# Kernel tuning notes

Measured on AMD Instinct MI355X. Metric: run time of the kernel, lower is better.

Reference implementation:

```python
import jax, jax.numpy as jnp
import numpy as np

HEAD_DIM = 64  # scale = head_dim ** -0.5


def setup_inputs() -> dict:
    key = jax.random.key(0)
    ks = jax.random.split(key, 5)
    B, S, E = 8, 8192, 1024
    L, D = 64, 256          # n_latent_vec, latent_dim
    H = HEAD_DIM
    return {
        "input_tensor": jax.random.normal(ks[0], (B, S, E), dtype=jnp.float32),
        "latents": jax.random.normal(ks[1], (L, D), dtype=jnp.float32),
        "Wq": jax.random.normal(ks[2], (H, D), dtype=jnp.float32) * (1.0 / np.sqrt(D)),
        "Wk": jax.random.normal(ks[3], (H, E), dtype=jnp.float32) * (1.0 / np.sqrt(E)),
        "Wv": jax.random.normal(ks[4], (H, E), dtype=jnp.float32) * (1.0 / np.sqrt(E)),
    }


def reference(input_tensor, latents, Wq, Wk, Wv):
    # non-cached path, seq_len == max_seq_len so no truncation
    # queries: broadcast shared latents over batch -> [B, L, H]
    q = jnp.einsum('ld,hd->lh', latents, Wq)                 # [L, H]
    k = jnp.einsum('bse,he->bsh', input_tensor, Wk)           # [B, S, H]
    v = jnp.einsum('bse,he->bsh', input_tensor, Wv)           # [B, S, H]
    scale = HEAD_DIM ** -0.5
    scores = jnp.einsum('lh,bsh->bls', q, k) * scale          # [B, L, S]
    weights = jax.nn.softmax(scores, axis=-1)                 # dropout is identity (p=0 / eval)
    out = jnp.einsum('bls,bsh->blh', weights, v)              # [B, L, H]
    return out
```

## Files before the change

kernel.cpp:

```cpp
#include <hip/hip_runtime.h>
#include <stdint.h>


typedef __attribute__((__ext_vector_type__(4))) float f32x4;
typedef __attribute__((__ext_vector_type__(8))) short bf16x8;

__device__ __forceinline__ unsigned short f2bf(float f) {
    union { float f; uint32_t u; } v; v.f = f;
    uint32_t u = v.u;
    return (unsigned short)((u + 0x7fffu + ((u >> 16) & 1u)) >> 16);
}

__device__ __forceinline__ unsigned long long pack4(f32x4 v) {
    return (unsigned long long)f2bf(v[0])        |
           ((unsigned long long)f2bf(v[1]) << 16) |
           ((unsigned long long)f2bf(v[2]) << 32) |
           ((unsigned long long)f2bf(v[3]) << 48);
}

__global__ __launch_bounds__(256) void prep_kernel(
    const float* __restrict__ latents, const float* __restrict__ Wq,
    const float* __restrict__ Wk, const float* __restrict__ Wv,
    unsigned short* __restrict__ wkv, unsigned short* __restrict__ qbf)
{
    const int blk = blockIdx.x, tid = threadIdx.x;
    if (blk < 128) {
        const float* src = (blk < 64) ? (Wk + (size_t)blk * 1024)
                                      : (Wv + (size_t)(blk - 64) * 1024);
        for (int i = tid; i < 1024; i += 256)
            wkv[(size_t)blk * 1024 + i] = f2bf(src[i]);
    } else {
        const int l = (blk - 128) * 4 + (tid >> 6);
        const int h = tid & 63;
        float a = 0.f;
        #pragma unroll 8
        for (int d = 0; d < 256; ++d)
            a += latents[l * 256 + d] * Wq[h * 256 + d];
        qbf[l * 64 + h] = f2bf(a * 0.125f);
    }
}

__global__ __launch_bounds__(512, 4) void fused_kernel(
    const float* __restrict__ x, const unsigned short* __restrict__ wkv,
    const unsigned short* __restrict__ qbf,
    float* __restrict__ Opart, float* __restrict__ mpart, float* __restrict__ spart)
{
    __shared__ unsigned short smem[33792];
    unsigned short* Ab = smem;
    unsigned short* Bb = smem + 10240;
    unsigned short* Cs = smem;
    unsigned short* qs = smem + 20480;
    unsigned short* Ps = smem + 25088;
    __shared__ float red[4][64];
    __shared__ float Mrow[64];

    const int tid = threadIdx.x;
    const int wave = tid >> 6, lane = tid & 63;
    const int g = lane >> 4, c = lane & 15;
    const int wr = wave >> 2, wc = wave & 3;
    const size_t r0 = (size_t)blockIdx.x * 128;

    {
        const int rowQ = tid >> 3, colQ = (tid & 7) * 8;
        *(uint4*)&qs[rowQ * 72 + colQ] = *(const uint4*)(qbf + rowQ * 64 + colQ);
    }

    const int rowA = tid >> 3, colA = (tid & 7) * 4;
    const int rowB = tid >> 2, colB = (tid & 3) * 8;

    f32x4 acc[4][2];
    #pragma unroll
    for (int i = 0; i < 4; ++i)
        #pragma unroll
        for (int j = 0; j < 2; ++j)
            acc[i][j] = f32x4{0.f, 0.f, 0.f, 0.f};

    f32x4 areg[2];
    uint4  breg;

    #pragma unroll
    for (int i = 0; i < 2; ++i)
        areg[i] = *(const f32x4*)(x + (r0 + rowA + 64 * i) * 1024 + colA);
    breg = *(const uint4*)(wkv + (size_t)rowB * 1024 + colB);
    #pragma unroll
    for (int i = 0; i < 2; ++i)
        *(unsigned long long*)&Ab[(rowA + 64 * i) * 40 + colA] = pack4(areg[i]);
    *(uint4*)&Bb[rowB * 40 + colB] = breg;
    __syncthreads();

    for (int t = 0; t < 32; ++t) {
        const int buf = t & 1;
        if (t < 31) {
            const int e0 = (t + 1) * 32;
            #pragma unroll
            for (int i = 0; i < 2; ++i)
                areg[i] = *(const f32x4*)(x + (r0 + rowA + 64 * i) * 1024 + e0 + colA);
            breg = *(const uint4*)(wkv + (size_t)rowB * 1024 + e0 + colB);
        }
        bf16x8 af[4], bfr[2];
        #pragma unroll
        for (int ml = 0; ml < 4; ++ml)
            af[ml] = *(const bf16x8*)&Ab[(buf * 128 + 64 * wr + 16 * ml + c) * 40 + 8 * g];
        #pragma unroll
        for (int nc = 0; nc < 2; ++nc)
            bfr[nc] = *(const bf16x8*)&Bb[(buf * 128 + 32 * wc + 16 * nc + c) * 40 + 8 * g];
        #pragma unroll
        for (int ml = 0; ml < 4; ++ml)
            #pragma unroll
            for (int nc = 0; nc < 2; ++nc)
                acc[ml][nc] = __builtin_amdgcn_mfma_f32_16x16x32_bf16(
                    af[ml], bfr[nc], acc[ml][nc], 0, 0, 0);
        if (t < 31) {
            const int nb = buf ^ 1;
            #pragma unroll
            for (int i = 0; i < 2; ++i)
                *(unsigned long long*)&Ab[(nb * 128 + rowA + 64 * i) * 40 + colA] =
                    pack4(areg[i]);
            *(uint4*)&Bb[(nb * 128 + rowB) * 40 + colB] = breg;
        }
        __syncthreads();
    }

    #pragma unroll
    for (int ml = 0; ml < 4; ++ml)
        #pragma unroll
        for (int nc = 0; nc < 2; ++nc)
            #pragma unroll
            for (int r = 0; r < 4; ++r)
                Cs[(64 * wr + 16 * ml + 4 * g + r) * 136 + 32 * wc + 16 * nc + c] =
                    f2bf(acc[ml][nc][r]);
    __syncthreads();

    f32x4 sc[4][2];
    if (wave < 4) {
        #pragma unroll
        for (int ml = 0; ml < 4; ++ml)
            #pragma unroll
            for (int ns = 0; ns < 2; ++ns)
                sc[ml][ns] = f32x4{0.f, 0.f, 0.f, 0.f};
        #pragma unroll
        for (int k0 = 0; k0 < 2; ++k0) {
            bf16x8 aq[4];
            #pragma unroll
            for (int ml = 0; ml < 4; ++ml)
                aq[ml] = *(const bf16x8*)&qs[(16 * ml + c) * 72 + 32 * k0 + 8 * g];
            #pragma unroll
            for (int ns = 0; ns < 2; ++ns) {
                bf16x8 bk = *(const bf16x8*)&Cs[(32 * wave + 16 * ns + c) * 136 + 32 * k0 + 8 * g];
                #pragma unroll
                for (int ml = 0; ml < 4; ++ml)
                    sc[ml][ns] = __builtin_amdgcn_mfma_f32_16x16x32_bf16(
                        aq[ml], bk, sc[ml][ns], 0, 0, 0);
            }
        }
        float mloc[4][4];
        #pragma unroll
        for (int ml = 0; ml < 4; ++ml)
            #pragma unroll
            for (int r = 0; r < 4; ++r)
                mloc[ml][r] = fmaxf(sc[ml][0][r], sc[ml][1][r]);
        #pragma unroll
        for (int off = 1; off <= 8; off <<= 1)
            #pragma unroll
            for (int ml = 0; ml < 4; ++ml)
                #pragma unroll
                for (int r = 0; r < 4; ++r)
                    mloc[ml][r] = fmaxf(mloc[ml][r], __shfl_xor(mloc[ml][r], off));
        if (c == 0)
            #pragma unroll
            for (int ml = 0; ml < 4; ++ml)
                #pragma unroll
                for (int r = 0; r < 4; ++r)
                    red[wave][16 * ml + 4 * g + r] = mloc[ml][r];
    }
    __syncthreads();
    if (tid < 64) {
        float m = red[0][tid];
        m = fmaxf(m, red[1][tid]); m = fmaxf(m, red[2][tid]); m = fmaxf(m, red[3][tid]);
        Mrow[tid] = m;
    }
    __syncthreads();

    if (wave < 4) {
        float ssum[4][4];
        #pragma unroll
        for (int ml = 0; ml < 4; ++ml)
            #pragma unroll
            for (int r = 0; r < 4; ++r)
                ssum[ml][r] = 0.f;
        #pragma unroll
        for (int ml = 0; ml < 4; ++ml)
            #pragma unroll
            for (int r = 0; r < 4; ++r) {
                const int l = 16 * ml + 4 * g + r;
                const float mr = Mrow[l];
                #pragma unroll
                for (int ns = 0; ns < 2; ++ns) {
                    float p = __expf(sc[ml][ns][r] - mr);
                    unsigned short pb = f2bf(p);
                    Ps[l * 136 + 32 * wave + 16 * ns + c] = pb;
                    union { uint32_t u; float f; } pv; pv.u = (uint32_t)pb << 16;
                    ssum[ml][r] += pv.f;
                }
            }
        #pragma unroll
        for (int off = 1; off <= 8; off <<= 1)
            #pragma unroll
            for (int ml = 0; ml < 4; ++ml)
                #pragma unroll
                for (int r = 0; r < 4; ++r)
                    ssum[ml][r] += __shfl_xor(ssum[ml][r], off);
        if (c == 0)
            #pragma unroll
            for (int ml = 0; ml < 4; ++ml)
                #pragma unroll
                for (int r = 0; r < 4; ++r)
                    red[wave][16 * ml + 4 * g + r] = ssum[ml][r];
    }
    __syncthreads();
    if (tid < 64) {
        const float s = red[0][tid] + red[1][tid] + red[2][tid] + red[3][tid];
        mpart[(size_t)blockIdx.x * 64 + tid] = Mrow[tid];
        spart[(size_t)blockIdx.x * 64 + tid] = s;
    }

    if (wave < 4) {
        f32x4 o[4];
        #pragma unroll
        for (int nh = 0; nh < 4; ++nh) o[nh] = f32x4{0.f, 0.f, 0.f, 0.f};
        #pragma unroll
        for (int ks = 0; ks < 4; ++ks) {
            bf16x8 ap = *(const bf16x8*)&Ps[(16 * wave + c) * 136 + 32 * ks + 8 * g];
            #pragma unroll
            for (int nh = 0; nh < 4; ++nh) {
                bf16x8 bv;
                #pragma unroll
                for (int j = 0; j < 8; ++j)
                    bv[j] = (short)Cs[(32 * ks + 8 * g + j) * 136 + 64 + 16 * nh + c];
                o[nh] = __builtin_amdgcn_mfma_f32_16x16x32_bf16(ap, bv, o[nh], 0, 0, 0);
            }
        }
        const size_t pb = (size_t)blockIdx.x * 64;
        #pragma unroll
        for (int nh = 0; nh < 4; ++nh)
            #pragma unroll
            for (int r = 0; r < 4; ++r) {
                const int l = 16 * wave + 4 * g + r;
                const int h = 16 * nh + c;
                Opart[(pb + l) * 64 + h] = o[nh][r];
            }
    }
}

__global__ __launch_bounds__(64) void combine_kernel(
    const float* __restrict__ Opart, const float* __restrict__ mpart,
    const float* __restrict__ spart, float* __restrict__ out)
{
    const int b = blockIdx.x >> 6, l = blockIdx.x & 63, h = threadIdx.x;
    float M = -3.0e38f;
    #pragma unroll 8
    for (int ch = 0; ch < 64; ++ch)
        M = fmaxf(M, mpart[((size_t)(b * 64 + ch)) * 64 + l]);
    float den = 0.f, acc = 0.f;
    #pragma unroll 8
    for (int ch = 0; ch < 64; ++ch) {
        const size_t idx = ((size_t)(b * 64 + ch)) * 64 + l;
        const float w = __expf(mpart[idx] - M);
        den += w * spart[idx];
        acc += w * Opart[idx * 64 + h];
    }
    out[((size_t)blockIdx.x) * 64 + h] = acc / den;
}

extern "C" void kernel_launch(void* const* d_in, const int* in_sizes, int n_in,
                              void* d_out, int out_size, void* d_ws, size_t ws_size,
                              hipStream_t stream)
{
    const float* x       = (const float*)d_in[0];
    const float* latents = (const float*)d_in[1];
    const float* Wq      = (const float*)d_in[2];
    const float* Wk      = (const float*)d_in[3];
    const float* Wv      = (const float*)d_in[4];
    float* out = (float*)d_out;
    char* ws = (char*)d_ws;

    unsigned short* wkv = (unsigned short*)(ws);
    unsigned short* qbf = (unsigned short*)(ws + 262144);
    float* Opart = (float*)(ws + 270336);
    float* mpart = (float*)(ws + 270336 + 8388608);
    float* spart = (float*)(ws + 270336 + 8388608 + 131072);

    hipLaunchKernelGGL(prep_kernel, dim3(144), dim3(256), 0, stream,
                       latents, Wq, Wk, Wv, wkv, qbf);
    hipLaunchKernelGGL(fused_kernel, dim3(512), dim3(512), 0, stream,
                       x, wkv, qbf, Opart, mpart, spart);
    hipLaunchKernelGGL(combine_kernel, dim3(512), dim3(64), 0, stream,
                       Opart, mpart, spart, out);
}
```

Measured before the change: 81.85 us.

## Halve fused block tile to 64 rows, read K/V weights directly from global

Each fused block now handles 64 sequence rows with 256 threads instead of 128 rows with 512 threads, which doubles the grid to 1024 blocks and the number of partial results the combine kernel merges. The bf16 Wk/Wv fragments are loaded straight from global memory (expected to hit cache) rather than staged through shared memory, and the K and V tiles are written into a shared buffer in two phases so shared memory shrinks sharply. The aim is higher occupancy and a better fill of the CUs, and all four waves now do useful work in the attention phase. In exchange, each block rereads the full weight matrix from cache, and the partial-result traffic and combine work double.

```diff
diff --git a/kernel.cpp b/kernel.cpp
--- a/kernel.cpp
+++ b/kernel.cpp
@@ -40,139 +40,121 @@
     }
 }
 
-__global__ __launch_bounds__(512, 4) void fused_kernel(
+__global__ __launch_bounds__(256, 4) void fused_kernel(
     const float* __restrict__ x, const unsigned short* __restrict__ wkv,
     const unsigned short* __restrict__ qbf,
     float* __restrict__ Opart, float* __restrict__ mpart, float* __restrict__ spart)
 {
-    __shared__ unsigned short smem[33792];
-    unsigned short* Ab = smem;
-    unsigned short* Bb = smem + 10240;
-    unsigned short* Cs = smem;
-    unsigned short* qs = smem + 20480;
-    unsigned short* Ps = smem + 25088;
+    __shared__ unsigned short smem[9856];
+    unsigned short* KV  = smem;
+    unsigned short* PsQ = smem + 4608;
+    unsigned short* Ab  = smem;
     __shared__ float red[4][64];
     __shared__ float Mrow[64];
 
     const int tid = threadIdx.x;
     const int wave = tid >> 6, lane = tid & 63;
     const int g = lane >> 4, c = lane & 15;
-    const int wr = wave >> 2, wc = wave & 3;
-    const size_t r0 = (size_t)blockIdx.x * 128;
-
-    {
-        const int rowQ = tid >> 3, colQ = (tid & 7) * 8;
-        *(uint4*)&qs[rowQ * 72 + colQ] = *(const uint4*)(qbf + rowQ * 64 + colQ);
-    }
-
-    const int rowA = tid >> 3, colA = (tid & 7) * 4;
-    const int rowB = tid >> 2, colB = (tid & 3) * 8;
-
-    f32x4 acc[4][2];
-    #pragma unroll
-    for (int i = 0; i < 4; ++i)
-        #pragma unroll
-        for (int j = 0; j < 2; ++j)
+    const int wr = wave >> 1, wc = wave & 1;
+    const size_t r0 = (size_t)blockIdx.x * 64;
+
+    const int rowS = tid >> 2, c4 = (tid & 3) * 4;
+
+    f32x4 acc[2][4];
+    #pragma unroll
+    for (int i = 0; i < 2; ++i)
+        #pragma unroll
+        for (int j = 0; j < 4; ++j)
             acc[i][j] = f32x4{0.f, 0.f, 0.f, 0.f};
 
-    f32x4 areg[2];
-    uint4  breg;
-
-    #pragma unroll
-    for (int i = 0; i < 2; ++i)
-        areg[i] = *(const f32x4*)(x + (r0 + rowA + 64 * i) * 1024 + colA);
-    breg = *(const uint4*)(wkv + (size_t)rowB * 1024 + colB);
-    #pragma unroll
-    for (int i = 0; i < 2; ++i)
-        *(unsigned long long*)&Ab[(rowA + 64 * i) * 40 + colA] = pack4(areg[i]);
-    *(uint4*)&Bb[rowB * 40 + colB] = breg;
+    f32x4 a0, a1;
+
+    a0 = *(const f32x4*)(x + (r0 + rowS) * 1024 + c4);
+    a1 = *(const f32x4*)(x + (r0 + rowS) * 1024 + c4 + 16);
+    *(unsigned long long*)&Ab[rowS * 40 + c4]      = pack4(a0);
+    *(unsigned long long*)&Ab[rowS * 40 + c4 + 16] = pack4(a1);
     __syncthreads();
 
     for (int t = 0; t < 32; ++t) {
         const int buf = t & 1;
         if (t < 31) {
             const int e0 = (t + 1) * 32;
-            #pragma unroll
-            for (int i = 0; i < 2; ++i)
-                areg[i] = *(const f32x4*)(x + (r0 + rowA + 64 * i) * 1024 + e0 + colA);
-            breg = *(const uint4*)(wkv + (size_t)rowB * 1024 + e0 + colB);
-        }
-        bf16x8 af[4], bfr[2];
-        #pragma unroll
-        for (int ml = 0; ml < 4; ++ml)
-            af[ml] = *(const bf16x8*)&Ab[(buf * 128 + 64 * wr + 16 * ml + c) * 40 + 8 * g];
-        #pragma unroll
-        for (int nc = 0; nc < 2; ++nc)
-            bfr[nc] = *(const bf16x8*)&Bb[(buf * 128 + 32 * wc + 16 * nc + c) * 40 + 8 * g];
-        #pragma unroll
-        for (int ml = 0; ml < 4; ++ml)
-            #pragma unroll
-            for (int nc = 0; nc < 2; ++nc)
+            a0 = *(const f32x4*)(x + (r0 + rowS) * 1024 + e0 + c4);
+            a1 = *(const f32x4*)(x + (r0 + rowS) * 1024 + e0 + c4 + 16);
+        }
+        bf16x8 br[4];
+        #pragma unroll
+        for (int nc = 0; nc < 4; ++nc)
+            br[nc] = *(const bf16x8*)(wkv + (size_t)(64 * wc + 16 * nc + c) * 1024
+                                      + 32 * t + 8 * g);
+        bf16x8 af[2];
+        #pragma unroll
+        for (int ml = 0; ml < 2; ++ml)
+            af[ml] = *(const bf16x8*)&Ab[(buf * 64 + 32 * wr + 16 * ml + c) * 40 + 8 * g];
+        #pragma unroll
+        for (int ml = 0; ml < 2; ++ml)
+            #pragma unroll
+            for (int nc = 0; nc < 4; ++nc)
                 acc[ml][nc] = __builtin_amdgcn_mfma_f32_16x16x32_bf16(
-                    af[ml], bfr[nc], acc[ml][nc], 0, 0, 0);
+                    af[ml], br[nc], acc[ml][nc], 0, 0, 0);
         if (t < 31) {
             const int nb = buf ^ 1;
-            #pragma unroll
-            for (int i = 0; i < 2; ++i)
-                *(unsigned long long*)&Ab[(nb * 128 + rowA + 64 * i) * 40 + colA] =
-                    pack4(areg[i]);
-            *(uint4*)&Bb[(nb * 128 + rowB) * 40 + colB] = breg;
+            *(unsigned long long*)&Ab[(nb * 64 + rowS) * 40 + c4]      = pack4(a0);
+            *(unsigned long long*)&Ab[(nb * 64 + rowS) * 40 + c4 + 16] = pack4(a1);
         }
         __syncthreads();
     }
 
-    #pragma unroll
-    for (int ml = 0; ml < 4; ++ml)
-        #pragma unroll
-        for (int nc = 0; nc < 2; ++nc)
-            #pragma unroll
-            for (int r = 0; r < 4; ++r)
-                Cs[(64 * wr + 16 * ml + 4 * g + r) * 136 + 32 * wc + 16 * nc + c] =
-                    f2bf(acc[ml][nc][r]);
-    __syncthreads();
-
-    f32x4 sc[4][2];
-    if (wave < 4) {
-        #pragma unroll
-        for (int ml = 0; ml < 4; ++ml)
-            #pragma unroll
-            for (int ns = 0; ns < 2; ++ns)
-                sc[ml][ns] = f32x4{0.f, 0.f, 0.f, 0.f};
-        #pragma unroll
-        for (int k0 = 0; k0 < 2; ++k0) {
-            bf16x8 aq[4];
-            #pragma unroll
-            for (int ml = 0; ml < 4; ++ml)
-                aq[ml] = *(const bf16x8*)&qs[(16 * ml + c) * 72 + 32 * k0 + 8 * g];
-            #pragma unroll
-            for (int ns = 0; ns < 2; ++ns) {
-                bf16x8 bk = *(const bf16x8*)&Cs[(32 * wave + 16 * ns + c) * 136 + 32 * k0 + 8 * g];
-                #pragma unroll
-                for (int ml = 0; ml < 4; ++ml)
-                    sc[ml][ns] = __builtin_amdgcn_mfma_f32_16x16x32_bf16(
-                        aq[ml], bk, sc[ml][ns], 0, 0, 0);
-            }
-        }
-        float mloc[4][4];
-        #pragma unroll
-        for (int ml = 0; ml < 4; ++ml)
-            #pragma unroll
-            for (int r = 0; r < 4; ++r)
-                mloc[ml][r] = fmaxf(sc[ml][0][r], sc[ml][1][r]);
-        #pragma unroll
-        for (int off = 1; off <= 8; off <<= 1)
-            #pragma unroll
-            for (int ml = 0; ml < 4; ++ml)
+    if (wc == 0)
+        #pragma unroll
+        for (int ml = 0; ml < 2; ++ml)
+            #pragma unroll
+            for (int nc = 0; nc < 4; ++nc)
                 #pragma unroll
                 for (int r = 0; r < 4; ++r)
-                    mloc[ml][r] = fmaxf(mloc[ml][r], __shfl_xor(mloc[ml][r], off));
-        if (c == 0)
-            #pragma unroll
-            for (int ml = 0; ml < 4; ++ml)
-                #pragma unroll
-                for (int r = 0; r < 4; ++r)
-                    red[wave][16 * ml + 4 * g + r] = mloc[ml][r];
-    }
+                    KV[(32 * wr + 16 * ml + 4 * g + r) * 72 + 16 * nc + c] =
+                        f2bf(acc[ml][nc][r]);
+    {
+        const int rowQ = tid >> 2, colQ = (tid & 3) * 8;
+        #pragma unroll
+        for (int j = 0; j < 2; ++j)
+            *(uint4*)&PsQ[rowQ * 72 + colQ + 32 * j] =
+                *(const uint4*)(qbf + rowQ * 64 + colQ + 32 * j);
+    }
+    __syncthreads();
+
+    f32x4 sc[4];
+    #pragma unroll
+    for (int ml = 0; ml < 4; ++ml) sc[ml] = f32x4{0.f, 0.f, 0.f, 0.f};
+    #pragma unroll
+    for (int k0 = 0; k0 < 2; ++k0) {
+        bf16x8 bk = *(const bf16x8*)&KV[(16 * wave + c) * 72 + 32 * k0 + 8 * g];
+        #pragma unroll
+        for (int ml = 0; ml < 4; ++ml) {
+            bf16x8 aq = *(const bf16x8*)&PsQ[(16 * ml + c) * 72 + 32 * k0 + 8 * g];
+            sc[ml] = __builtin_amdgcn_mfma_f32_16x16x32_bf16(aq, bk, sc[ml], 0, 0, 0);
+        }
+    }
+
+    float mloc[4][4];
+    #pragma unroll
+    for (int ml = 0; ml < 4; ++ml)
+        #pragma unroll
+        for (int r = 0; r < 4; ++r)
+            mloc[ml][r] = sc[ml][r];
+    #pragma unroll
+    for (int off = 1; off <= 8; off <<= 1)
+        #pragma unroll
+        for (int ml = 0; ml < 4; ++ml)
+            #pragma unroll
+            for (int r = 0; r < 4; ++r)
+                mloc[ml][r] = fmaxf(mloc[ml][r], __shfl_xor(mloc[ml][r], off));
+    if (c == 0)
+        #pragma unroll
+        for (int ml = 0; ml < 4; ++ml)
+            #pragma unroll
+            for (int r = 0; r < 4; ++r)
+                red[wave][16 * ml + 4 * g + r] = mloc[ml][r];
     __syncthreads();
     if (tid < 64) {
         float m = red[0][tid];
@@ -181,42 +163,40 @@
     }
     __syncthreads();
 
-    if (wave < 4) {
-        float ssum[4][4];
-        #pragma unroll
-        for (int ml = 0; ml < 4; ++ml)
-            #pragma unroll
-            for (int r = 0; r < 4; ++r)
-                ssum[ml][r] = 0.f;
-        #pragma unroll
-        for (int ml = 0; ml < 4; ++ml)
-            #pragma unroll
-            for (int r = 0; r < 4; ++r) {
-                const int l = 16 * ml + 4 * g + r;
-                const float mr = Mrow[l];
-                #pragma unroll
-                for (int ns = 0; ns < 2; ++ns) {
-                    float p = __expf(sc[ml][ns][r] - mr);
-                    unsigned short pb = f2bf(p);
-                    Ps[l * 136 + 32 * wave + 16 * ns + c] = pb;
-                    union { uint32_t u; float f; } pv; pv.u = (uint32_t)pb << 16;
-                    ssum[ml][r] += pv.f;
-                }
-            }
-        #pragma unroll
-        for (int off = 1; off <= 8; off <<= 1)
-            #pragma unroll
-            for (int ml = 0; ml < 4; ++ml)
+    if (wc == 1)
+        #pragma unroll
+        for (int ml = 0; ml < 2; ++ml)
+            #pragma unroll
+            for (int nc = 0; nc < 4; ++nc)
                 #pragma unroll
                 for (int r = 0; r < 4; ++r)
-                    ssum[ml][r] += __shfl_xor(ssum[ml][r], off);
-        if (c == 0)
-            #pragma unroll
-            for (int ml = 0; ml < 4; ++ml)
-                #pragma unroll
-                for (int r = 0; r < 4; ++r)
-                    red[wave][16 * ml + 4 * g + r] = ssum[ml][r];
-    }
+                    KV[(32 * wr + 16 * ml + 4 * g + r) * 72 + 16 * nc + c] =
+                        f2bf(acc[ml][nc][r]);
+    float ssum[4][4];
+    #pragma unroll
+    for (int ml = 0; ml < 4; ++ml)
+        #pragma unroll
+        for (int r = 0; r < 4; ++r) {
+            const int l = 16 * ml + 4 * g + r;
+            float p = __expf(sc[ml][r] - Mrow[l]);
+            unsigned short pb = f2bf(p);
+            PsQ[l * 72 + 16 * wave + c] = pb;
+            union { uint32_t u; float f; } pv; pv.u = (uint32_t)pb << 16;
+            ssum[ml][r] = pv.f;
+        }
+    #pragma unroll
+    for (int off = 1; off <= 8; off <<= 1)
+        #pragma unroll
+        for (int ml = 0; ml < 4; ++ml)
+            #pragma unroll
+            for (int r = 0; r < 4; ++r)
+                ssum[ml][r] += __shfl_xor(ssum[ml][r], off);
+    if (c == 0)
+        #pragma unroll
+        for (int ml = 0; ml < 4; ++ml)
+            #pragma unroll
+            for (int r = 0; r < 4; ++r)
+                red[wave][16 * ml + 4 * g + r] = ssum[ml][r];
     __syncthreads();
     if (tid < 64) {
         const float s = red[0][tid] + red[1][tid] + red[2][tid] + red[3][tid];
@@ -224,32 +204,30 @@
         spart[(size_t)blockIdx.x * 64 + tid] = s;
     }
 
-    if (wave < 4) {
-        f32x4 o[4];
-        #pragma unroll
-        for (int nh = 0; nh < 4; ++nh) o[nh] = f32x4{0.f, 0.f, 0.f, 0.f};
-        #pragma unroll
-        for (int ks = 0; ks < 4; ++ks) {
-            bf16x8 ap = *(const bf16x8*)&Ps[(16 * wave + c) * 136 + 32 * ks + 8 * g];
-            #pragma unroll
-            for (int nh = 0; nh < 4; ++nh) {
-                bf16x8 bv;
-                #pragma unroll
-                for (int j = 0; j < 8; ++j)
-                    bv[j] = (short)Cs[(32 * ks + 8 * g + j) * 136 + 64 + 16 * nh + c];
-                o[nh] = __builtin_amdgcn_mfma_f32_16x16x32_bf16(ap, bv, o[nh], 0, 0, 0);
-            }
-        }
-        const size_t pb = (size_t)blockIdx.x * 64;
-        #pragma unroll
-        for (int nh = 0; nh < 4; ++nh)
-            #pragma unroll
-            for (int r = 0; r < 4; ++r) {
-                const int l = 16 * wave + 4 * g + r;
-                const int h = 16 * nh + c;
-                Opart[(pb + l) * 64 + h] = o[nh][r];
-            }
-    }
+    f32x4 o[4];
+    #pragma unroll
+    for (int nh = 0; nh < 4; ++nh) o[nh] = f32x4{0.f, 0.f, 0.f, 0.f};
+    #pragma unroll
+    for (int ks = 0; ks < 2; ++ks) {
+        bf16x8 ap = *(const bf16x8*)&PsQ[(16 * wave + c) * 72 + 32 * ks + 8 * g];
+        #pragma unroll
+        for (int nh = 0; nh < 4; ++nh) {
+            bf16x8 bv;
+            #pragma unroll
+            for (int j = 0; j < 8; ++j)
+                bv[j] = (short)KV[(32 * ks + 8 * g + j) * 72 + 16 * nh + c];
+            o[nh] = __builtin_amdgcn_mfma_f32_16x16x32_bf16(ap, bv, o[nh], 0, 0, 0);
+        }
+    }
+    const size_t pb = (size_t)blockIdx.x * 64;
+    #pragma unroll
+    for (int nh = 0; nh < 4; ++nh)
+        #pragma unroll
+        for (int r = 0; r < 4; ++r) {
+            const int l = 16 * wave + 4 * g + r;
+            const int h = 16 * nh + c;
+            Opart[(pb + l) * 64 + h] = o[nh][r];
+        }
 }
 
 __global__ __launch_bounds__(64) void combine_kernel(
@@ -259,12 +237,12 @@
     const int b = blockIdx.x >> 6, l = blockIdx.x & 63, h = threadIdx.x;
     float M = -3.0e38f;
     #pragma unroll 8
-    for (int ch = 0; ch < 64; ++ch)
-        M = fmaxf(M, mpart[((size_t)(b * 64 + ch)) * 64 + l]);
+    for (int ch = 0; ch < 128; ++ch)
+        M = fmaxf(M, mpart[((size_t)(b * 128 + ch)) * 64 + l]);
     float den = 0.f, acc = 0.f;
     #pragma unroll 8
-    for (int ch = 0; ch < 64; ++ch) {
-        const size_t idx = ((size_t)(b * 64 + ch)) * 64 + l;
+    for (int ch = 0; ch < 128; ++ch) {
+        const size_t idx = ((size_t)(b * 128 + ch)) * 64 + l;
         const float w = __expf(mpart[idx] - M);
         den += w * spart[idx];
         acc += w * Opart[idx * 64 + h];
@@ -287,12 +265,12 @@
     unsigned short* wkv = (unsigned short*)(ws);
     unsigned short* qbf = (unsigned short*)(ws + 262144);
     float* Opart = (float*)(ws + 270336);
-    float* mpart = (float*)(ws + 270336 + 8388608);
-    float* spart = (float*)(ws + 270336 + 8388608 + 131072);
+    float* mpart = (float*)(ws + 270336 + 16777216);
+    float* spart = (float*)(ws + 270336 + 16777216 + 262144);
 
     hipLaunchKernelGGL(prep_kernel, dim3(144), dim3(256), 0, stream,
                        latents, Wq, Wk, Wv, wkv, qbf);
-    hipLaunchKernelGGL(fused_kernel, dim3(512), dim3(512), 0, stream,
+    hipLaunchKernelGGL(fused_kernel, dim3(1024), dim3(256), 0, stream,
                        x, wkv, qbf, Opart, mpart, spart);
     hipLaunchKernelGGL(combine_kernel, dim3(512), dim3(64), 0, stream,
                        Opart, mpart, spart, out);
```

After: 139.0 us. 1.7x slower.
